# Performance work log

Measured on AMD Instinct MI355X. Metric: run time of the kernel, lower is better.

## Reference

```python
import jax, jax.numpy as jnp
import numpy as np


def setup_inputs() -> dict:
    key = jax.random.key(0)
    ks = jax.random.split(key, 8)
    B, C, H, W = 4, 256, 64, 64
    x = jax.random.normal(ks[0], (B, C, H, W), dtype=jnp.float32)
    y = jax.random.normal(ks[1], (B, C, H, W), dtype=jnp.float32)
    s = 1.0 / np.sqrt(C)
    Wq = jax.random.normal(ks[2], (C, C), dtype=jnp.float32) * s
    bq = jax.random.normal(ks[3], (C,), dtype=jnp.float32) * 0.02
    Wk = jax.random.normal(ks[4], (C, C), dtype=jnp.float32) * s
    bk = jax.random.normal(ks[5], (C,), dtype=jnp.float32) * 0.02
    Wv = jax.random.normal(ks[6], (C, C), dtype=jnp.float32) * s
    bv = jax.random.normal(ks[7], (C,), dtype=jnp.float32) * 0.02
    return {"x": x, "y": y, "Wq": Wq, "bq": bq, "Wk": Wk, "bk": bk, "Wv": Wv, "bv": bv}


def reference(x, y, Wq, bq, Wk, bk, Wv, bv):
    B, C, H, W = x.shape
    scale = C ** (-0.5)
    # flatten spatial dims: [B, N, C] with N = H*W
    x_flat = x.reshape(B, C, H * W).transpose(0, 2, 1)
    y_flat = y.reshape(B, C, H * W).transpose(0, 2, 1)
    # linear projections (torch Linear: x @ W.T + b)
    Q = jnp.einsum('bnc,dc->bnd', x_flat, Wq) + bq
    K = jnp.einsum('bnc,dc->bnd', y_flat, Wk) + bk
    V = jnp.einsum('bnc,dc->bnd', y_flat, Wv) + bv
    # single-head full cross-attention
    scores = jnp.einsum('bqd,bkd->bqk', Q, K) * scale  # [B, N, N]
    attn = jax.nn.softmax(scores, axis=-1)
    out = jnp.einsum('bqk,bkd->bqd', attn, V)  # [B, N, C]
    out = out.transpose(0, 2, 1).reshape(B, C, H, W)
    return x + out
```

## Files before the change

kernel.cpp:

```cpp
#include <hip/hip_runtime.h>
#include <stdint.h>

#define BN 4
#define CD 256
#define ND 4096
#define NK 32

typedef unsigned short u16;
typedef short bfrag __attribute__((ext_vector_type(8)));
typedef float ffrag __attribute__((ext_vector_type(4)));

__device__ __forceinline__ float bf2f(u16 u) {
  union { unsigned int i; float f; } v;
  v.i = ((unsigned int)u) << 16;
  return v.f;
}
__device__ __forceinline__ u16 f2bf(float f) {
  union { float f; unsigned int i; } v;
  v.f = f;
  return (u16)((v.i + 0x7FFFu + ((v.i >> 16) & 1u)) >> 16);
}
__device__ __forceinline__ void gload_lds(const u16* g, u16* l) {
  __builtin_amdgcn_global_load_lds(
      (const __attribute__((address_space(1))) void*)g,
      (__attribute__((address_space(3))) void*)l, 16, 0, 0);
}

__global__ __launch_bounds__(256) void k_cvtW(
    const float* __restrict__ Wq, const float* __restrict__ Wk,
    const float* __restrict__ Wv, u16* __restrict__ wb) {
  int m = blockIdx.y;
  const float* src = (m == 0) ? Wq : ((m == 1) ? Wk : Wv);
  u16* dst = wb + (size_t)m * CD * CD;
  int i = (blockIdx.x * 256 + threadIdx.x) * 4;
  float4 v = *(const float4*)(src + i);
  ushort4 o;
  o.x = f2bf(v.x); o.y = f2bf(v.y); o.z = f2bf(v.z); o.w = f2bf(v.w);
  *(ushort4*)(dst + i) = o;
}

__global__ __launch_bounds__(256) void k_transpose(
    const float* __restrict__ x, const float* __restrict__ y,
    u16* __restrict__ xT, u16* __restrict__ yT) {
  __shared__ alignas(16) u16 tile[64][72];
  int n0 = blockIdx.x * 64, c0 = blockIdx.y * 64, bz = blockIdx.z;
  const float* src = (bz < BN) ? x : y;
  u16* dst = (bz < BN) ? xT : yT;
  int b = bz & (BN - 1);
  src += (size_t)b * CD * ND;
  dst += (size_t)b * ND * CD;
  int t = threadIdx.x;
#pragma unroll
  for (int it = 0; it < 4; ++it) {
    int idx = it * 256 + t;
    int ci = idx >> 4;
    int nj = (idx & 15) * 4;
    float4 v = *(const float4*)(src + (size_t)(c0 + ci) * ND + n0 + nj);
    tile[nj + 0][ci] = f2bf(v.x);
    tile[nj + 1][ci] = f2bf(v.y);
    tile[nj + 2][ci] = f2bf(v.z);
    tile[nj + 3][ci] = f2bf(v.w);
  }
  __syncthreads();
#pragma unroll
  for (int it = 0; it < 2; ++it) {
    int idx = it * 256 + t;
    int ni = idx >> 3;
    int cj = (idx & 7) * 8;
    uint4 v = *(const uint4*)&tile[ni][cj];
    *(uint4*)(dst + (size_t)(n0 + ni) * CD + c0 + cj) = v;
  }
}

__global__ __launch_bounds__(256, 2) void k_proj(
    const u16* __restrict__ A, const u16* __restrict__ Bw,
    const float* __restrict__ biasA, const float* __restrict__ biasB,
    u16* __restrict__ C, int ldc, int bias_per_row,
    size_t aBS, size_t bBS, size_t cBS) {
  __shared__ alignas(16) u16 As[64][264];
  __shared__ alignas(16) u16 Bs[64][136];
  int m0 = blockIdx.x * 64, n0 = blockIdx.y * 64;
  size_t z = blockIdx.z;
  const float* bias = (z == 0) ? biasA : biasB;
  A += z * aBS; Bw += z * bBS; C += z * cBS;
  int t = threadIdx.x, w = t >> 6, l = t & 63;
  int lane16 = l & 15, quad = l >> 4;
#pragma unroll
  for (int it = 0; it < 8; ++it) {
    int c = it * 256 + t;
    int r = c >> 5, co = (c & 31) * 8;
    *(uint4*)&As[r][co] = *(const uint4*)(A + (size_t)(m0 + r) * CD + co);
  }
  ffrag acc[4];
#pragma unroll
  for (int tt = 0; tt < 4; ++tt) acc[tt] = ffrag{0.f, 0.f, 0.f, 0.f};
#pragma unroll
  for (int half = 0; half < 2; ++half) {
    if (half) __syncthreads();
#pragma unroll
    for (int it = 0; it < 4; ++it) {
      int c = it * 256 + t;
      int r = c >> 4, co = (c & 15) * 8;
      *(uint4*)&Bs[r][co] =
          *(const uint4*)(Bw + (size_t)(n0 + r) * CD + half * 128 + co);
    }
    __syncthreads();
#pragma unroll
    for (int kc = 0; kc < 4; ++kc) {
      bfrag af = *(const bfrag*)&As[w * 16 + lane16][half * 128 + kc * 32 + quad * 8];
#pragma unroll
      for (int tt = 0; tt < 4; ++tt) {
        bfrag bfr = *(const bfrag*)&Bs[tt * 16 + lane16][kc * 32 + quad * 8];
        acc[tt] = __builtin_amdgcn_mfma_f32_16x16x32_bf16(af, bfr, acc[tt], 0, 0, 0);
      }
    }
  }
#pragma unroll
  for (int tt = 0; tt < 4; ++tt) {
    int col = n0 + tt * 16 + lane16;
    float bcol = bias_per_row ? 0.f : bias[col];
#pragma unroll
    for (int r = 0; r < 4; ++r) {
      int row = m0 + w * 16 + quad * 4 + r;
      float bb = bias_per_row ? bias[row] : bcol;
      C[(size_t)row * ldc + col] = f2bf(acc[tt][r] + bb);
    }
  }
}

union SmemU {
  struct {
    u16 Ks[2][NK][256];
    u16 Vs[2][CD][NK];
    u16 Ps[8][16][40];
  } a;
  u16 ot[CD][136];
};

template <int NS>
__global__ __launch_bounds__(256, 2) void k_attn(
    const u16* __restrict__ Q, const u16* __restrict__ K,
    const u16* __restrict__ Vt, u16* __restrict__ O01,
    u16* __restrict__ O23, float* __restrict__ Lpart) {
  constexpr int NIT = ND / NS / NK;
  __shared__ alignas(16) SmemU sm;
  int b = blockIdx.y, q0 = blockIdx.x * 128, z = blockIdx.z;
  int t = threadIdx.x, w = t >> 6, l = t & 63;
  int lane16 = l & 15, quad = l >> 4;
  const float scale = 0.0625f;

  bfrag qf[2][8];
#pragma unroll
  for (int mi = 0; mi < 2; ++mi) {
    const u16* Qrow =
        Q + ((size_t)b * ND + q0 + (w * 2 + mi) * 16 + lane16) * CD;
#pragma unroll
    for (int kc = 0; kc < 8; ++kc)
      qf[mi][kc] = *(const bfrag*)(Qrow + kc * 32 + quad * 8);
  }

  ffrag o[2][16];
#pragma unroll
  for (int mi = 0; mi < 2; ++mi)
#pragma unroll
    for (int i = 0; i < 16; ++i) o[mi][i] = ffrag{0.f, 0.f, 0.f, 0.f};
  float lsum[2][4] = {{0.f, 0.f, 0.f, 0.f}, {0.f, 0.f, 0.f, 0.f}};

  const u16* Kb = K + ((size_t)b * ND + z * (ND / NS)) * CD;
  const u16* Vb = Vt + (size_t)b * CD * ND + z * (ND / NS);

  auto stage = [&](int kt2) {
    int dbuf = kt2 & 1;
    const u16* Kt = Kb + (size_t)kt2 * NK * CD;
    const u16* Vtt = Vb + kt2 * NK;
#pragma unroll
    for (int p = 0; p < 4; ++p) {
      int r = p * 8 + w * 2 + (l >> 5);
      int j = (l & 31) ^ (r & 7);
      gload_lds(Kt + (size_t)r * CD + j * 8, &sm.a.Ks[dbuf][p * 8 + w * 2][0]);
    }
#pragma unroll
    for (int p = 0; p < 4; ++p) {
      int dd = p * 64 + w * 16 + (l >> 2);
      int j = (l & 3) ^ ((dd >> 1) & 3);
      gload_lds(Vtt + (size_t)dd * ND + j * 8, &sm.a.Vs[dbuf][p * 64 + w * 16][0]);
    }
  };

  stage(0);
  for (int kt = 0; kt < NIT; ++kt) {
    int dbuf = kt & 1;
    __syncthreads();
    if (kt + 1 < NIT) stage(kt + 1);

    ffrag s2[2][2];
#pragma unroll
    for (int mi = 0; mi < 2; ++mi)
#pragma unroll
      for (int tt = 0; tt < 2; ++tt) s2[mi][tt] = ffrag{0.f, 0.f, 0.f, 0.f};
#pragma unroll
    for (int kc = 0; kc < 8; ++kc) {
      bfrag kf0, kf1;
      {
        int r = lane16;
        int cp = (kc * 4 + quad) ^ (r & 7);
        kf0 = *(const bfrag*)&sm.a.Ks[dbuf][r][cp * 8];
        int r1 = 16 + lane16;
        int cp1 = (kc * 4 + quad) ^ (r1 & 7);
        kf1 = *(const bfrag*)&sm.a.Ks[dbuf][r1][cp1 * 8];
      }
#pragma unroll
      for (int mi = 0; mi < 2; ++mi) {
        s2[mi][0] = __builtin_amdgcn_mfma_f32_16x16x32_bf16(qf[mi][kc], kf0,
                                                            s2[mi][0], 0, 0, 0);
        s2[mi][1] = __builtin_amdgcn_mfma_f32_16x16x32_bf16(qf[mi][kc], kf1,
                                                            s2[mi][1], 0, 0, 0);
      }
    }

#pragma unroll
    for (int mi = 0; mi < 2; ++mi)
#pragma unroll
      for (int tt = 0; tt < 2; ++tt)
#pragma unroll
        for (int r = 0; r < 4; ++r) {
          float p = __expf(s2[mi][tt][r] * scale);
          lsum[mi][r] += p;
          sm.a.Ps[w * 2 + mi][quad * 4 + r][tt * 16 + lane16] = f2bf(p);
        }
    bfrag pf0 = *(const bfrag*)&sm.a.Ps[w * 2 + 0][lane16][quad * 8];
    bfrag pf1 = *(const bfrag*)&sm.a.Ps[w * 2 + 1][lane16][quad * 8];

#pragma unroll
    for (int dt = 0; dt < 16; ++dt) {
      int dd = dt * 16 + lane16;
      int cp = quad ^ ((dd >> 1) & 3);
      bfrag vf = *(const bfrag*)&sm.a.Vs[dbuf][dd][cp * 8];
      o[0][dt] = __builtin_amdgcn_mfma_f32_16x16x32_bf16(pf0, vf, o[0][dt], 0, 0, 0);
      o[1][dt] = __builtin_amdgcn_mfma_f32_16x16x32_bf16(pf1, vf, o[1][dt], 0, 0, 0);
    }
  }

#pragma unroll
  for (int mi = 0; mi < 2; ++mi)
#pragma unroll
    for (int r = 0; r < 4; ++r) {
#pragma unroll
      for (int off = 1; off < 16; off <<= 1)
        lsum[mi][r] += __shfl_xor(lsum[mi][r], off, 64);
    }
  if (lane16 == 0) {
#pragma unroll
    for (int mi = 0; mi < 2; ++mi)
#pragma unroll
      for (int r = 0; r < 4; ++r)
        Lpart[((size_t)z * BN + b) * ND + q0 + (w * 2 + mi) * 16 + quad * 4 + r] =
            lsum[mi][r];
  }

  __syncthreads();
#pragma unroll
  for (int mi = 0; mi < 2; ++mi)
#pragma unroll
    for (int dt = 0; dt < 16; ++dt)
#pragma unroll
      for (int r = 0; r < 4; ++r)
        sm.ot[dt * 16 + lane16][(w * 2 + mi) * 16 + quad * 4 + r] =
            f2bf(o[mi][dt][r]);
  __syncthreads();
  const size_t SZc = (size_t)BN * ND * CD;
  u16* Op = ((z < 2) ? O01 : O23) + (size_t)(z & 1) * SZc;
#pragma unroll
  for (int it = 0; it < 16; ++it) {
    int c = it * 256 + t;
    int dd = c >> 4, co = (c & 15) * 8;
    size_t g = ((size_t)b * CD + dd) * ND + q0 + co;
    *(uint4*)(Op + g) = *(const uint4*)&sm.ot[dd][co];
  }
}

template <int NS>
__global__ __launch_bounds__(256) void k_combine(
    const u16* __restrict__ O01, const u16* __restrict__ O23,
    const float* __restrict__ L, const float* __restrict__ x,
    float* __restrict__ out) {
  const size_t SZc = (size_t)BN * ND * CD;
  size_t e = ((size_t)blockIdx.x * 256 + threadIdx.x) * 8;
  int n = (int)(e & (ND - 1));
  int b = (int)(e >> 20);
  float ls[8] = {0, 0, 0, 0, 0, 0, 0, 0};
  float acc[8] = {0, 0, 0, 0, 0, 0, 0, 0};
#pragma unroll
  for (int z = 0; z < NS; ++z) {
    const float* Lr = L + ((size_t)z * BN + b) * ND + n;
    float4 l0 = *(const float4*)(Lr);
    float4 l1 = *(const float4*)(Lr + 4);
    ls[0] += l0.x; ls[1] += l0.y; ls[2] += l0.z; ls[3] += l0.w;
    ls[4] += l1.x; ls[5] += l1.y; ls[6] += l1.z; ls[7] += l1.w;
    const u16* Oz = ((z < 2) ? O01 : O23) + (size_t)(z & 1) * SZc + e;
    union { uint4 q; u16 s[8]; } u;
    u.q = *(const uint4*)Oz;
#pragma unroll
    for (int j = 0; j < 8; ++j) acc[j] += bf2f(u.s[j]);
  }
  float4 x0 = *(const float4*)(x + e);
  float4 x1 = *(const float4*)(x + e + 4);
  float4 r0, r1;
  r0.x = x0.x + acc[0] / ls[0];
  r0.y = x0.y + acc[1] / ls[1];
  r0.z = x0.z + acc[2] / ls[2];
  r0.w = x0.w + acc[3] / ls[3];
  r1.x = x1.x + acc[4] / ls[4];
  r1.y = x1.y + acc[5] / ls[5];
  r1.z = x1.z + acc[6] / ls[6];
  r1.w = x1.w + acc[7] / ls[7];
  *(float4*)(out + e) = r0;
  *(float4*)(out + e + 4) = r1;
}

extern "C" void kernel_launch(void* const* d_in, const int* in_sizes, int n_in,
                              void* d_out, int out_size, void* d_ws, size_t ws_size,
                              hipStream_t stream) {
  const float* x  = (const float*)d_in[0];
  const float* y  = (const float*)d_in[1];
  const float* Wq = (const float*)d_in[2];
  const float* bq = (const float*)d_in[3];
  const float* Wk = (const float*)d_in[4];
  const float* bk = (const float*)d_in[5];
  const float* Wv = (const float*)d_in[6];
  const float* bv = (const float*)d_in[7];
  float* out = (float*)d_out;
  u16* ws = (u16*)d_ws;
  const size_t WSZ = (size_t)3 * CD * CD;
  const size_t SZ  = (size_t)BN * ND * CD;
  u16* wB = ws;
  u16* xT = ws + WSZ;
  u16* yT = xT + SZ;
  u16* Qb = yT + SZ;
  u16* Kb = Qb + SZ;
  u16* Vb = Kb + SZ;
  u16* O23 = Vb + SZ;
  u16* O01 = xT;
  float* Lp = (float*)ws;
  const size_t need4 = (WSZ + 7 * SZ) * sizeof(u16);
  const bool big = ws_size >= need4;
  const int cgrid = (int)(SZ / (256 * 8));

  k_cvtW<<<dim3(64, 3), 256, 0, stream>>>(Wq, Wk, Wv, wB);
  k_transpose<<<dim3(ND / 64, CD / 64, BN * 2), 256, 0, stream>>>(x, y, xT, yT);
  k_proj<<<dim3(BN * ND / 64, CD / 64, 2), 256, 0, stream>>>(
      xT, wB, bq, bk, Qb, CD, 0, SZ, (size_t)CD * CD, SZ);
  k_proj<<<dim3(CD / 64, ND / 64, BN), 256, 0, stream>>>(
      wB + (size_t)2 * CD * CD, yT, bv, bv, Vb, ND, 1,
      (size_t)0, (size_t)ND * CD, (size_t)CD * ND);
  if (big) {
    k_attn<4><<<dim3(ND / 128, BN, 4), 256, 0, stream>>>(Qb, Kb, Vb, O01, O23, Lp);
    k_combine<4><<<dim3(cgrid), 256, 0, stream>>>(O01, O23, Lp, x, out);
  } else {
    k_attn<2><<<dim3(ND / 128, BN, 2), 256, 0, stream>>>(Qb, Kb, Vb, O01, O01, Lp);
    k_combine<2><<<dim3(cgrid), 256, 0, stream>>>(O01, O01, Lp, x, out);
  }
}
```

Baseline: 206.8 us.

## Fuse weight conversion and input transpose into projection GEMM kernels

The separate weight-to-bf16 conversion and the x/y transpose kernels are removed. The Q/K projection now reads fp32 x/y directly and transposes them into LDS while converting to bf16. The V projection does the same for y, and both kernels convert the fp32 weights on the fly. This drops two launches and the round trip of the bf16 xT/yT intermediates through global memory. In exchange, fp32 inputs and weights are re-read by several blocks, and the transposed LDS stores may cause bank conflicts. The workspace layout is also reorganised to match.

```diff
diff --git a/kernel.cpp b/kernel.cpp
--- a/kernel.cpp
+++ b/kernel.cpp
@@ -26,71 +26,35 @@
       (__attribute__((address_space(3))) void*)l, 16, 0, 0);
 }
 
-__global__ __launch_bounds__(256) void k_cvtW(
+__global__ __launch_bounds__(256, 2) void k_projQK(
+    const float* __restrict__ x, const float* __restrict__ y,
     const float* __restrict__ Wq, const float* __restrict__ Wk,
-    const float* __restrict__ Wv, u16* __restrict__ wb) {
-  int m = blockIdx.y;
-  const float* src = (m == 0) ? Wq : ((m == 1) ? Wk : Wv);
-  u16* dst = wb + (size_t)m * CD * CD;
-  int i = (blockIdx.x * 256 + threadIdx.x) * 4;
-  float4 v = *(const float4*)(src + i);
-  ushort4 o;
-  o.x = f2bf(v.x); o.y = f2bf(v.y); o.z = f2bf(v.z); o.w = f2bf(v.w);
-  *(ushort4*)(dst + i) = o;
-}
-
-__global__ __launch_bounds__(256) void k_transpose(
-    const float* __restrict__ x, const float* __restrict__ y,
-    u16* __restrict__ xT, u16* __restrict__ yT) {
-  __shared__ alignas(16) u16 tile[64][72];
-  int n0 = blockIdx.x * 64, c0 = blockIdx.y * 64, bz = blockIdx.z;
-  const float* src = (bz < BN) ? x : y;
-  u16* dst = (bz < BN) ? xT : yT;
-  int b = bz & (BN - 1);
-  src += (size_t)b * CD * ND;
-  dst += (size_t)b * ND * CD;
-  int t = threadIdx.x;
-#pragma unroll
-  for (int it = 0; it < 4; ++it) {
-    int idx = it * 256 + t;
-    int ci = idx >> 4;
-    int nj = (idx & 15) * 4;
-    float4 v = *(const float4*)(src + (size_t)(c0 + ci) * ND + n0 + nj);
-    tile[nj + 0][ci] = f2bf(v.x);
-    tile[nj + 1][ci] = f2bf(v.y);
-    tile[nj + 2][ci] = f2bf(v.z);
-    tile[nj + 3][ci] = f2bf(v.w);
-  }
-  __syncthreads();
-#pragma unroll
-  for (int it = 0; it < 2; ++it) {
-    int idx = it * 256 + t;
-    int ni = idx >> 3;
-    int cj = (idx & 7) * 8;
-    uint4 v = *(const uint4*)&tile[ni][cj];
-    *(uint4*)(dst + (size_t)(n0 + ni) * CD + c0 + cj) = v;
-  }
-}
-
-__global__ __launch_bounds__(256, 2) void k_proj(
-    const u16* __restrict__ A, const u16* __restrict__ Bw,
-    const float* __restrict__ biasA, const float* __restrict__ biasB,
-    u16* __restrict__ C, int ldc, int bias_per_row,
-    size_t aBS, size_t bBS, size_t cBS) {
+    const float* __restrict__ bq, const float* __restrict__ bk,
+    u16* __restrict__ Qb, u16* __restrict__ Kb) {
   __shared__ alignas(16) u16 As[64][264];
   __shared__ alignas(16) u16 Bs[64][136];
-  int m0 = blockIdx.x * 64, n0 = blockIdx.y * 64;
-  size_t z = blockIdx.z;
-  const float* bias = (z == 0) ? biasA : biasB;
-  A += z * aBS; Bw += z * bBS; C += z * cBS;
+  int n0 = blockIdx.x * 64;
+  int m0 = blockIdx.y * 64;
+  int z = blockIdx.z;
+  int b = m0 >> 12, nsp = m0 & 4095;
+  const float* src = (z ? y : x) + (size_t)b * CD * ND;
+  const float* Wsrc = (z ? Wk : Wq) + (size_t)n0 * CD;
+  const float* bias = (z ? bk : bq) + n0;
+  u16* Cd = (z ? Kb : Qb) + (size_t)m0 * CD + n0;
   int t = threadIdx.x, w = t >> 6, l = t & 63;
   int lane16 = l & 15, quad = l >> 4;
-#pragma unroll
-  for (int it = 0; it < 8; ++it) {
-    int c = it * 256 + t;
-    int r = c >> 5, co = (c & 31) * 8;
-    *(uint4*)&As[r][co] = *(const uint4*)(A + (size_t)(m0 + r) * CD + co);
-  }
+
+#pragma unroll
+  for (int it = 0; it < 16; ++it) {
+    int idx = it * 256 + t;
+    int c = idx >> 4, nj = (idx & 15) * 4;
+    float4 v = *(const float4*)(src + (size_t)c * ND + nsp + nj);
+    As[nj + 0][c] = f2bf(v.x);
+    As[nj + 1][c] = f2bf(v.y);
+    As[nj + 2][c] = f2bf(v.z);
+    As[nj + 3][c] = f2bf(v.w);
+  }
+
   ffrag acc[4];
 #pragma unroll
   for (int tt = 0; tt < 4; ++tt) acc[tt] = ffrag{0.f, 0.f, 0.f, 0.f};
@@ -98,11 +62,13 @@
   for (int half = 0; half < 2; ++half) {
     if (half) __syncthreads();
 #pragma unroll
-    for (int it = 0; it < 4; ++it) {
-      int c = it * 256 + t;
-      int r = c >> 4, co = (c & 15) * 8;
-      *(uint4*)&Bs[r][co] =
-          *(const uint4*)(Bw + (size_t)(n0 + r) * CD + half * 128 + co);
+    for (int it = 0; it < 8; ++it) {
+      int idx = it * 256 + t;
+      int row = idx >> 5, cj = (idx & 31) * 4;
+      float4 v = *(const float4*)(Wsrc + (size_t)row * CD + half * 128 + cj);
+      ushort4 o;
+      o.x = f2bf(v.x); o.y = f2bf(v.y); o.z = f2bf(v.z); o.w = f2bf(v.w);
+      *(ushort4*)&Bs[row][cj] = o;
     }
     __syncthreads();
 #pragma unroll
@@ -117,13 +83,73 @@
   }
 #pragma unroll
   for (int tt = 0; tt < 4; ++tt) {
-    int col = n0 + tt * 16 + lane16;
-    float bcol = bias_per_row ? 0.f : bias[col];
+    int colL = tt * 16 + lane16;
+    float bcol = bias[colL];
 #pragma unroll
     for (int r = 0; r < 4; ++r) {
-      int row = m0 + w * 16 + quad * 4 + r;
-      float bb = bias_per_row ? bias[row] : bcol;
-      C[(size_t)row * ldc + col] = f2bf(acc[tt][r] + bb);
+      int rowL = w * 16 + quad * 4 + r;
+      Cd[(size_t)rowL * CD + colL] = f2bf(acc[tt][r] + bcol);
+    }
+  }
+}
+
+__global__ __launch_bounds__(256, 2) void k_projV(
+    const float* __restrict__ y, const float* __restrict__ Wv,
+    const float* __restrict__ bv, u16* __restrict__ Vb) {
+  __shared__ alignas(16) u16 As[64][264];
+  __shared__ alignas(16) u16 Bs[64][136];
+  int n0s = blockIdx.x * 64;
+  int m0 = blockIdx.y * 64;
+  int b = blockIdx.z;
+  const float* Bsrc = y + (size_t)b * CD * ND + n0s;
+  u16* Cd = Vb + ((size_t)b * CD + m0) * ND + n0s;
+  int t = threadIdx.x, w = t >> 6, l = t & 63;
+  int lane16 = l & 15, quad = l >> 4;
+
+#pragma unroll
+  for (int it = 0; it < 16; ++it) {
+    int idx = it * 256 + t;
+    int row = idx >> 6, cj = (idx & 63) * 4;
+    float4 v = *(const float4*)(Wv + (size_t)(m0 + row) * CD + cj);
+    ushort4 o;
+    o.x = f2bf(v.x); o.y = f2bf(v.y); o.z = f2bf(v.z); o.w = f2bf(v.w);
+    *(ushort4*)&As[row][cj] = o;
+  }
+
+  ffrag acc[4];
+#pragma unroll
+  for (int tt = 0; tt < 4; ++tt) acc[tt] = ffrag{0.f, 0.f, 0.f, 0.f};
+#pragma unroll
+  for (int half = 0; half < 2; ++half) {
+    if (half) __syncthreads();
+#pragma unroll
+    for (int it = 0; it < 8; ++it) {
+      int idx = it * 256 + t;
+      int cl = idx >> 4, nj = (idx & 15) * 4;
+      float4 v = *(const float4*)(Bsrc + (size_t)(half * 128 + cl) * ND + nj);
+      Bs[nj + 0][cl] = f2bf(v.x);
+      Bs[nj + 1][cl] = f2bf(v.y);
+      Bs[nj + 2][cl] = f2bf(v.z);
+      Bs[nj + 3][cl] = f2bf(v.w);
+    }
+    __syncthreads();
+#pragma unroll
+    for (int kc = 0; kc < 4; ++kc) {
+      bfrag af = *(const bfrag*)&As[w * 16 + lane16][half * 128 + kc * 32 + quad * 8];
+#pragma unroll
+      for (int tt = 0; tt < 4; ++tt) {
+        bfrag bfr = *(const bfrag*)&Bs[tt * 16 + lane16][kc * 32 + quad * 8];
+        acc[tt] = __builtin_amdgcn_mfma_f32_16x16x32_bf16(af, bfr, acc[tt], 0, 0, 0);
+      }
+    }
+  }
+#pragma unroll
+  for (int tt = 0; tt < 4; ++tt) {
+    int colL = tt * 16 + lane16;
+#pragma unroll
+    for (int r = 0; r < 4; ++r) {
+      int rowL = w * 16 + quad * 4 + r;
+      Cd[(size_t)rowL * ND + colL] = f2bf(acc[tt][r] + bv[m0 + rowL]);
     }
   }
 }
@@ -331,33 +357,25 @@
   const float* bv = (const float*)d_in[7];
   float* out = (float*)d_out;
   u16* ws = (u16*)d_ws;
-  const size_t WSZ = (size_t)3 * CD * CD;
-  const size_t SZ  = (size_t)BN * ND * CD;
-  u16* wB = ws;
-  u16* xT = ws + WSZ;
-  u16* yT = xT + SZ;
-  u16* Qb = yT + SZ;
+  const size_t SZ = (size_t)BN * ND * CD;
+  u16* Qb = ws;
   u16* Kb = Qb + SZ;
   u16* Vb = Kb + SZ;
-  u16* O23 = Vb + SZ;
-  u16* O01 = xT;
-  float* Lp = (float*)ws;
-  const size_t need4 = (WSZ + 7 * SZ) * sizeof(u16);
+  u16* Ob = Vb + SZ;
+  const size_t need4 = 7 * SZ * sizeof(u16) + (size_t)4 * BN * ND * sizeof(float);
   const bool big = ws_size >= need4;
   const int cgrid = (int)(SZ / (256 * 8));
 
-  k_cvtW<<<dim3(64, 3), 256, 0, stream>>>(Wq, Wk, Wv, wB);
-  k_transpose<<<dim3(ND / 64, CD / 64, BN * 2), 256, 0, stream>>>(x, y, xT, yT);
-  k_proj<<<dim3(BN * ND / 64, CD / 64, 2), 256, 0, stream>>>(
-      xT, wB, bq, bk, Qb, CD, 0, SZ, (size_t)CD * CD, SZ);
-  k_proj<<<dim3(CD / 64, ND / 64, BN), 256, 0, stream>>>(
-      wB + (size_t)2 * CD * CD, yT, bv, bv, Vb, ND, 1,
-      (size_t)0, (size_t)ND * CD, (size_t)CD * ND);
+  k_projQK<<<dim3(4, 256, 2), 256, 0, stream>>>(x, y, Wq, Wk, bq, bk, Qb, Kb);
+  k_projV<<<dim3(64, 4, 4), 256, 0, stream>>>(y, Wv, bv, Vb);
   if (big) {
-    k_attn<4><<<dim3(ND / 128, BN, 4), 256, 0, stream>>>(Qb, Kb, Vb, O01, O23, Lp);
-    k_combine<4><<<dim3(cgrid), 256, 0, stream>>>(O01, O23, Lp, x, out);
+    float* Lp = (float*)(Ob + 4 * SZ);
+    k_attn<4><<<dim3(ND / 128, BN, 4), 256, 0, stream>>>(Qb, Kb, Vb, Ob,
+                                                         Ob + 2 * SZ, Lp);
+    k_combine<4><<<dim3(cgrid), 256, 0, stream>>>(Ob, Ob + 2 * SZ, Lp, x, out);
   } else {
-    k_attn<2><<<dim3(ND / 128, BN, 2), 256, 0, stream>>>(Qb, Kb, Vb, O01, O01, Lp);
-    k_combine<2><<<dim3(cgrid), 256, 0, stream>>>(O01, O01, Lp, x, out);
-  }
-}
+    float* Lp = (float*)(Ob + 2 * SZ);
+    k_attn<2><<<dim3(ND / 128, BN, 2), 256, 0, stream>>>(Qb, Kb, Vb, Ob, Ob, Lp);
+    k_combine<2><<<dim3(cgrid), 256, 0, stream>>>(Ob, Ob, Lp, x, out);
+  }
+}
```

Result: slower. 211.8 us (+2.4%).
